# Kernel optimization log

Measured on AMD Instinct MI355X. Metric: run time of the kernel, lower is better.

Reference implementation:

```python
import jax, jax.numpy as jnp
import numpy as np

EMB = 1024
SHARED_MLP = 2048
MOE_MLP = 1024
N_EXPERTS = 8
TOP_K = 2
EPS = 1e-6


def rms_norm(x, scale=None, eps=EPS):
    # MaxText RMSNorm: x * rsqrt(mean(x^2)+eps) [* scale]
    y = x * jax.lax.rsqrt(jnp.mean(jnp.square(x), axis=-1, keepdims=True) + eps)
    return y if scale is None else y * scale


def setup_inputs() -> dict:
    key = jax.random.key(0)
    ks = jax.random.split(key, 12)
    B, S, D, F, M, E = 2, 2048, EMB, SHARED_MLP, MOE_MLP, N_EXPERTS
    sd = D ** -0.5
    sm = M ** -0.5
    sf = F ** -0.5
    return {
        "inputs": jax.random.normal(ks[0], (B, S, D), jnp.float32),
        "original_inputs": jax.random.normal(ks[1], (B, S, D), jnp.float32),
        # norm scales (init ~ ones with small perturbation for non-trivial math)
        "pre_forward_scale": 1.0 + 0.02 * jax.random.normal(ks[2], (D,), jnp.float32),
        "pre_ff_ln2_scale": 1.0 + 0.02 * jax.random.normal(ks[3], (D,), jnp.float32),
        "post_ff_ln1_scale": 1.0 + 0.02 * jax.random.normal(ks[4], (D,), jnp.float32),
        "post_ff_ln2_scale": 1.0 + 0.02 * jax.random.normal(ks[5], (D,), jnp.float32),
        # router and routed expert weights
        "router_w": jax.random.normal(ks[6], (D, E), jnp.float32) * sd,
        "e_wi0": jax.random.normal(ks[7], (E, D, M), jnp.float32) * sd,
        "e_wi1": jax.random.normal(ks[8], (E, D, M), jnp.float32) * sd,
        "e_wo": jax.random.normal(ks[9], (E, M, D), jnp.float32) * sm,
        # shared expert (gated MLP)
        "s_wi0": jax.random.normal(ks[10], (D, F), jnp.float32) * sd,
        "s_wi1": jax.random.normal(ks[11], (D, F), jnp.float32) * sd,
        "s_wo": jax.random.normal(jax.random.fold_in(key, 99), (F, D), jnp.float32) * sf,
    }


def _forward(inputs, original_inputs, pre_forward_scale, pre_ff_ln2_scale,
             post_ff_ln1_scale, post_ff_ln2_scale, router_w,
             e_wi0, e_wi1, e_wo, s_wi0, s_wi1, s_wo):
    B, S, D = inputs.shape
    E, K = N_EXPERTS, TOP_K
    # ---- shared experts: gated GeLU MLP on `inputs` ----
    h_sh = jax.nn.gelu(jnp.einsum('bsd,df->bsf', inputs, s_wi0)) * \
           jnp.einsum('bsd,df->bsf', inputs, s_wi1)
    shared = jnp.einsum('bsf,fd->bsd', h_sh, s_wo)
    shared = rms_norm(shared, post_ff_ln1_scale)
    # ---- gate-norm scaling (no-scale RMSNorm * emb^-0.5 * learned scale) ----
    routed_in = rms_norm(original_inputs, pre_ff_ln2_scale)
    gate_in = rms_norm(original_inputs) * (D ** -0.5) * pre_forward_scale  # f32 gate
    # ---- routing: softmax logits, top-k, renormalized combine weights ----
    logits = jnp.einsum('bsd,de->bse', gate_in.astype(jnp.float32), router_w)
    probs = jax.nn.softmax(logits, axis=-1)                       # [B,S,E]
    top_w, top_i = jax.lax.top_k(probs, K)                        # [B,S,K]
    top_w = top_w / jnp.sum(top_w, axis=-1, keepdims=True)
    onehot = jax.nn.one_hot(top_i, E, dtype=probs.dtype)          # [B,S,K,E]
    combine = jnp.einsum('bske,bsk->bse', onehot, top_w)          # [B,S,E]
    # ---- dropless routed experts: dense per-expert gated FFN + weighted combine ----
    x = routed_in.reshape(B * S, D)                               # [T,D]
    cw = combine.reshape(B * S, E)                                # [T,E]
    h = jax.nn.gelu(jnp.einsum('td,edm->etm', x, e_wi0)) * \
        jnp.einsum('td,edm->etm', x, e_wi1)                       # [E,T,M]
    routed = jnp.einsum('etm,emd,te->td', h, e_wo, cw)            # [T,D]
    routed = rms_norm(routed.reshape(B, S, D), post_ff_ln2_scale)
    # ---- load-balance aux loss (switch-style) ----
    frac_tokens = jnp.mean(jnp.sum(onehot, axis=-2), axis=(0, 1)) / K  # [E]
    frac_probs = jnp.mean(probs, axis=(0, 1))                          # [E]
    lb_loss = E * jnp.sum(frac_tokens * frac_probs)
    return routed + shared, lb_loss


def reference(inputs, original_inputs, pre_forward_scale, pre_ff_ln2_scale,
              post_ff_ln1_scale, post_ff_ln2_scale, router_w,
              e_wi0, e_wi1, e_wo, s_wi0, s_wi1, s_wo):
    out, lb_loss = _forward(inputs, original_inputs, pre_forward_scale,
                            pre_ff_ln2_scale, post_ff_ln1_scale, post_ff_ln2_scale,
                            router_w, e_wi0, e_wi1, e_wo, s_wi0, s_wi1, s_wo)
    return out, lb_loss
```

## Files before the change

kernel.cpp:

```cpp
#include <hip/hip_runtime.h>
#include <stdint.h>


typedef unsigned short u16;
typedef u16 u16x4 __attribute__((ext_vector_type(4)));
typedef u16 u16x8 __attribute__((ext_vector_type(8)));
typedef _Float16 f16x8 __attribute__((ext_vector_type(8)));
typedef float f32x4 __attribute__((ext_vector_type(4)));
typedef __attribute__((address_space(1))) void* as1_vp;
typedef __attribute__((address_space(3))) void* as3_vp;

#define T_TOK 4096
#define DIM   1024
#define FDIM  2048
#define MDIM  1024
#define NEXP  8
#define MAXTILES 72
#define HROWS (MAXTILES * 128)

__device__ __forceinline__ u16 f2h(float f) {
  _Float16 h = (_Float16)f;
  return __builtin_bit_cast(u16, h);
}
__device__ __forceinline__ float h2f(u16 u) {
  return (float)__builtin_bit_cast(_Float16, u);
}
__device__ __forceinline__ float gelu_f(float x) {
  const float y2 = x * (1.5957691216f + 0.0713548163f * x * x);
  return x / (1.0f + __expf(-y2));
}
__device__ __forceinline__ void async_copy16(const void* g, void* l) {
  __builtin_amdgcn_global_load_lds((as1_vp)(uintptr_t)g,
                                   (as3_vp)(uint32_t)(uintptr_t)l, 16, 0, 0);
}
__device__ __forceinline__ f16x8 lds_frag(const u16* p) {
  return __builtin_bit_cast(f16x8, *(const u16x8*)p);
}

__global__ __launch_bounds__(256, 2) void gemm_in(
    const u16* __restrict__ xs, const u16* __restrict__ swi_t,
    const u16* __restrict__ routed, const u16* __restrict__ ewi_t,
    u16* __restrict__ Hs, u16* __restrict__ Hr,
    const int* __restrict__ ridx, const int2* __restrict__ tdesc,
    const int* __restrict__ n_tiles) {
  const int yb = (int)blockIdx.y;
  const u16 *A, *B0t, *B1t;
  u16* H;
  int N;
  long bm;
  bool gather;
  if (yb < 32) {
    bm = (long)yb * 128;
    A = xs;
    B0t = swi_t;
    B1t = swi_t + (size_t)FDIM * DIM;
    H = Hs;
    N = FDIM;
    gather = false;
  } else {
    const int ty = yb - 32;
    if (ty >= *n_tiles) return;
    if ((int)blockIdx.x >= MDIM / 128) return;
    const int2 td = tdesc[ty];
    bm = td.y;
    A = routed;
    B0t = ewi_t + (long)td.x * MDIM * DIM;
    B1t = ewi_t + (size_t)NEXP * MDIM * DIM + (long)td.x * MDIM * DIM;
    H = Hr;
    N = MDIM;
    gather = true;
  }
  __shared__ __align__(16) u16 As[128 * 64];
  __shared__ __align__(16) u16 Bs0[128 * 64];
  __shared__ __align__(16) u16 Bs1[128 * 64];
  const int tid = threadIdx.x;
  const int lane = tid & 63;
  const int wave = tid >> 6;
  const int wm = (wave >> 1) * 64;
  const int wn = (wave & 1) * 64;
  const long bn = (long)blockIdx.x * 128;

  f32x4 acc0[4][4] = {}, acc1[4][4] = {};

  const int r0 = tid >> 3;
  const int cc = ((tid & 7) ^ (r0 & 7)) * 8;
  const long rowstride = 32 * (long)DIM;
  const u16* Ag[4];
  if (gather) {
#pragma unroll
    for (int i = 0; i < 4; i++) Ag[i] = A + (long)ridx[bm + r0 + i * 32] * DIM + cc;
  } else {
#pragma unroll
    for (int i = 0; i < 4; i++) Ag[i] = A + (bm + r0 + i * 32) * (long)DIM + cc;
  }
  const u16* B0g = B0t + (bn + r0) * (long)DIM + cc;
  const u16* B1g = B1t + (bn + r0) * (long)DIM + cc;
  const int fr = lane & 15;
  const int fq = lane >> 4;

  for (int k0 = 0; k0 < DIM; k0 += 64) {
#pragma unroll
    for (int i = 0; i < 4; i++) {
      async_copy16(Ag[i] + k0, &As[tid * 8 + i * 2048]);
      async_copy16(B0g + i * rowstride + k0, &Bs0[tid * 8 + i * 2048]);
      async_copy16(B1g + i * rowstride + k0, &Bs1[tid * 8 + i * 2048]);
    }
    __syncthreads();
#pragma unroll
    for (int kc = 0; kc < 8; kc += 4) {
      f16x8 af[4], b0[4], b1[4];
      const int q = (fq + kc) ^ (fr & 7);
#pragma unroll
      for (int i = 0; i < 4; i++) {
        af[i] = lds_frag(&As[(wm + i * 16 + fr) * 64 + q * 8]);
        b0[i] = lds_frag(&Bs0[(wn + i * 16 + fr) * 64 + q * 8]);
        b1[i] = lds_frag(&Bs1[(wn + i * 16 + fr) * 64 + q * 8]);
      }
#pragma unroll
      for (int mi = 0; mi < 4; mi++)
#pragma unroll
        for (int ni = 0; ni < 4; ni++) {
          acc0[mi][ni] = __builtin_amdgcn_mfma_f32_16x16x32_f16(af[mi], b0[ni], acc0[mi][ni], 0, 0, 0);
          acc1[mi][ni] = __builtin_amdgcn_mfma_f32_16x16x32_f16(af[mi], b1[ni], acc1[mi][ni], 0, 0, 0);
        }
    }
    __syncthreads();
  }

  const int er = (lane >> 4) * 4;
  const int ec = lane & 15;
#pragma unroll
  for (int mi = 0; mi < 4; mi++)
#pragma unroll
    for (int r = 0; r < 4; r++) {
      const long row = bm + wm + mi * 16 + er + r;
#pragma unroll
      for (int ni = 0; ni < 4; ni++)
        H[row * N + bn + wn + ni * 16 + ec] =
            f2h(gelu_f(acc0[mi][ni][r]) * acc1[mi][ni][r]);
    }
}

__global__ __launch_bounds__(256) void gemm_out2(
    const u16* __restrict__ Hs, const u16* __restrict__ swo_t,
    float* __restrict__ racc, const u16* __restrict__ Hr,
    const u16* __restrict__ ewo_t, float* __restrict__ Hout,
    const int2* __restrict__ tdesc, const int* __restrict__ n_tiles) {
  const int yb = (int)blockIdx.y;
  const u16 *A, *Bt;
  float* C;
  long bm;
  int K;
  if (yb < 32) {
    bm = (long)yb * 128;
    A = Hs;
    Bt = swo_t;
    K = FDIM;
    C = racc;
  } else {
    const int ty = yb - 32;
    if (ty >= *n_tiles) return;
    const int2 td = tdesc[ty];
    bm = td.y;
    A = Hr;
    Bt = ewo_t + (long)td.x * DIM * MDIM;
    K = MDIM;
    C = Hout;
  }
  __shared__ __align__(16) u16 As[128 * 64];
  __shared__ __align__(16) u16 Bs[128 * 64];
  const int tid = threadIdx.x;
  const int lane = tid & 63;
  const int wave = tid >> 6;
  const int wm = (wave >> 1) * 64;
  const int wn = (wave & 1) * 64;
  const long bn = (long)blockIdx.x * 128;

  f32x4 acc[4][4] = {};
  const int r0 = tid >> 3;
  const int cc = ((tid & 7) ^ (r0 & 7)) * 8;
  const long rowstride = 32 * (long)K;
  const u16* Ag[4];
#pragma unroll
  for (int i = 0; i < 4; i++) Ag[i] = A + (bm + r0 + i * 32) * (long)K + cc;
  const u16* Bg = Bt + (bn + r0) * (long)K + cc;
  const int fr = lane & 15;
  const int fq = lane >> 4;

  for (int k0 = 0; k0 < K; k0 += 64) {
#pragma unroll
    for (int i = 0; i < 4; i++) {
      async_copy16(Ag[i] + k0, &As[tid * 8 + i * 2048]);
      async_copy16(Bg + i * rowstride + k0, &Bs[tid * 8 + i * 2048]);
    }
    __syncthreads();
#pragma unroll
    for (int kc = 0; kc < 8; kc += 4) {
      f16x8 af[4], bq[4];
      const int q = (fq + kc) ^ (fr & 7);
#pragma unroll
      for (int i = 0; i < 4; i++) {
        af[i] = lds_frag(&As[(wm + i * 16 + fr) * 64 + q * 8]);
        bq[i] = lds_frag(&Bs[(wn + i * 16 + fr) * 64 + q * 8]);
      }
#pragma unroll
      for (int mi = 0; mi < 4; mi++)
#pragma unroll
        for (int ni = 0; ni < 4; ni++)
          acc[mi][ni] = __builtin_amdgcn_mfma_f32_16x16x32_f16(af[mi], bq[ni], acc[mi][ni], 0, 0, 0);
    }
    __syncthreads();
  }

  const int er = (lane >> 4) * 4;
  const int ec = lane & 15;
#pragma unroll
  for (int mi = 0; mi < 4; mi++)
#pragma unroll
    for (int r = 0; r < 4; r++) {
      const long row = bm + wm + mi * 16 + er + r;
#pragma unroll
      for (int ni = 0; ni < 4; ni++)
        C[row * DIM + bn + wn + ni * 16 + ec] = acc[mi][ni][r];
    }
}

__global__ __launch_bounds__(256) void transpose_cvt2(
    const float* __restrict__ s0, const float* __restrict__ s1,
    u16* __restrict__ dst, int R, int C, int zsplit) {
  __shared__ float tile[64][65];
  const int z = blockIdx.z;
  const float* src = (z < zsplit) ? s0 + (size_t)z * R * C
                                  : s1 + (size_t)(z - zsplit) * R * C;
  u16* d = dst + (size_t)z * R * C;
  const int c0 = blockIdx.x * 64, r0 = blockIdx.y * 64;
  const int tx = (threadIdx.x & 15) * 4;
  const int ty = threadIdx.x >> 4;
#pragma unroll
  for (int p = 0; p < 4; p++) {
    const float4 v =
        *(const float4*)(src + (size_t)(r0 + ty + p * 16) * C + c0 + tx);
    tile[ty + p * 16][tx + 0] = v.x;
    tile[ty + p * 16][tx + 1] = v.y;
    tile[ty + p * 16][tx + 2] = v.z;
    tile[ty + p * 16][tx + 3] = v.w;
  }
  __syncthreads();
  const int or8 = (threadIdx.x & 7) * 8;
  const int oc = threadIdx.x >> 3;
#pragma unroll
  for (int p = 0; p < 2; p++) {
    const int c = oc + p * 32;
    u16x8 o;
#pragma unroll
    for (int j = 0; j < 8; j++) o[j] = f2h(tile[or8 + j][c]);
    *(u16x8*)(d + (size_t)(c0 + c) * R + r0 + or8) = o;
  }
}

__global__ __launch_bounds__(256) void router_kernel(
    const float* __restrict__ orig, const float* __restrict__ inputs,
    const float* __restrict__ pfs, const float* __restrict__ ln2s,
    const float* __restrict__ rw, u16* __restrict__ routed_in,
    u16* __restrict__ x_sh, int* __restrict__ eidx, float* __restrict__ ewt,
    float* __restrict__ probs_out) {
  const int t = blockIdx.x;
  const int tid = threadIdx.x;
  const int d = tid * 4;
  {
    const float4 xi = *(const float4*)(inputs + (long)t * DIM + d);
    u16x4 xo = {f2h(xi.x), f2h(xi.y), f2h(xi.z), f2h(xi.w)};
    *(u16x4*)(x_sh + (long)t * DIM + d) = xo;
  }
  const float4 v = *(const float4*)(orig + (long)t * DIM + d);
  float ss = v.x * v.x + v.y * v.y + v.z * v.z + v.w * v.w;
#pragma unroll
  for (int off = 32; off > 0; off >>= 1) ss += __shfl_down(ss, off);
  __shared__ float red[4];
  __shared__ float lred[4][8];
  if ((tid & 63) == 0) red[tid >> 6] = ss;
  __syncthreads();
  const float rs = rsqrtf((red[0] + red[1] + red[2] + red[3]) * (1.0f / DIM) + 1e-6f);

  const float4 l2 = *(const float4*)(ln2s + d);
  u16x4 ro = {f2h(v.x * rs * l2.x), f2h(v.y * rs * l2.y), f2h(v.z * rs * l2.z),
              f2h(v.w * rs * l2.w)};
  *(u16x4*)(routed_in + (long)t * DIM + d) = ro;

  const float4 pf = *(const float4*)(pfs + d);
  const float c = rs * 0.03125f;
  const float g0 = v.x * c * pf.x, g1 = v.y * c * pf.y;
  const float g2 = v.z * c * pf.z, g3 = v.w * c * pf.w;
  float lg[8];
#pragma unroll
  for (int e = 0; e < 8; e++)
    lg[e] = g0 * rw[(d + 0) * 8 + e] + g1 * rw[(d + 1) * 8 + e] +
            g2 * rw[(d + 2) * 8 + e] + g3 * rw[(d + 3) * 8 + e];
#pragma unroll
  for (int e = 0; e < 8; e++)
#pragma unroll
    for (int off = 32; off > 0; off >>= 1) lg[e] += __shfl_down(lg[e], off);
  if ((tid & 63) == 0)
#pragma unroll
    for (int e = 0; e < 8; e++) lred[tid >> 6][e] = lg[e];
  __syncthreads();
  if (tid == 0) {
    float lz[8], p[8];
    float mx = -1e30f;
#pragma unroll
    for (int e = 0; e < 8; e++) {
      lz[e] = lred[0][e] + lred[1][e] + lred[2][e] + lred[3][e];
      mx = fmaxf(mx, lz[e]);
    }
    float s = 0.0f;
#pragma unroll
    for (int e = 0; e < 8; e++) {
      p[e] = expf(lz[e] - mx);
      s += p[e];
    }
    const float invs = 1.0f / s;
#pragma unroll
    for (int e = 0; e < 8; e++) p[e] *= invs;
    int i1 = 0;
    for (int e = 1; e < 8; e++)
      if (p[e] > p[i1]) i1 = e;
    int i2 = (i1 == 0) ? 1 : 0;
    for (int e = 0; e < 8; e++)
      if (e != i1 && p[e] > p[i2]) i2 = e;
    const float wsum = p[i1] + p[i2];
    eidx[2 * t] = i1;
    eidx[2 * t + 1] = i2;
    ewt[2 * t] = p[i1] / wsum;
    ewt[2 * t + 1] = p[i2] / wsum;
    float* prow = probs_out + (long)t * 8;
    for (int e = 0; e < 8; e++) prow[e] = p[e];
  }
}

__global__ __launch_bounds__(256) void bucket_count(const int* __restrict__ eidx,
                                                    int* __restrict__ counts) {
  __shared__ int lcnt[8];
  const int tid = threadIdx.x;
  if (tid < 8) lcnt[tid] = 0;
  __syncthreads();
  const int t = blockIdx.x * 256 + tid;
  atomicAdd(&lcnt[eidx[2 * t]], 1);
  atomicAdd(&lcnt[eidx[2 * t + 1]], 1);
  __syncthreads();
  if (tid < 8) atomicAdd(&counts[tid], lcnt[tid]);
}

__global__ void setup_tiles(const int* __restrict__ counts, int* __restrict__ poffset,
                            int2* __restrict__ tdesc, int* __restrict__ n_tiles) {
  if (threadIdx.x == 0 && blockIdx.x == 0) {
    int cur = 0, nt = 0;
    for (int e = 0; e < NEXP; e++) {
      poffset[e] = cur;
      const int ntile = (counts[e] + 127) >> 7;
      for (int i = 0; i < ntile; i++) {
        int2 d;
        d.x = e;
        d.y = cur + i * 128;
        tdesc[nt++] = d;
      }
      cur += ntile * 128;
    }
    n_tiles[0] = nt;
  }
}

__global__ __launch_bounds__(256) void bucket_scatter(
    const int* __restrict__ eidx, const int* __restrict__ poffset,
    int* __restrict__ cursors, int* __restrict__ ridx, int* __restrict__ pos) {
  __shared__ int lcnt[8], base[8];
  const int tid = threadIdx.x;
  if (tid < 8) lcnt[tid] = 0;
  __syncthreads();
  const int t = blockIdx.x * 256 + tid;
  const int e0 = eidx[2 * t], e1 = eidx[2 * t + 1];
  const int r0 = atomicAdd(&lcnt[e0], 1);
  const int r1 = atomicAdd(&lcnt[e1], 1);
  __syncthreads();
  if (tid < 8) base[tid] = atomicAdd(&cursors[tid], lcnt[tid]);
  __syncthreads();
  const int p0 = poffset[e0] + base[e0] + r0;
  const int p1 = poffset[e1] + base[e1] + r1;
  ridx[p0] = t;
  ridx[p1] = t;
  pos[2 * t] = p0;
  pos[2 * t + 1] = p1;
}

__global__ __launch_bounds__(256) void lb_reduce(const float* __restrict__ probs,
                                                 const int* __restrict__ counts,
                                                 float* __restrict__ out) {
  const int tid = threadIdx.x;
  float psum[8] = {};
  for (int tt = 0; tt < 16; tt++) {
    const long t = (long)tid * 16 + tt;
    const float4* pp = (const float4*)(probs + t * 8);
    const float4 p0 = pp[0], p1 = pp[1];
    psum[0] += p0.x; psum[1] += p0.y; psum[2] += p0.z; psum[3] += p0.w;
    psum[4] += p1.x; psum[5] += p1.y; psum[6] += p1.z; psum[7] += p1.w;
  }
#pragma unroll
  for (int e = 0; e < 8; e++)
#pragma unroll
    for (int off = 32; off > 0; off >>= 1) psum[e] += __shfl_down(psum[e], off);
  __shared__ float sp[4][8];
  if ((tid & 63) == 0)
#pragma unroll
    for (int e = 0; e < 8; e++) sp[tid >> 6][e] = psum[e];
  __syncthreads();
  if (tid == 0) {
    float loss = 0.0f;
#pragma unroll
    for (int e = 0; e < 8; e++) {
      const float fp = (sp[0][e] + sp[1][e] + sp[2][e] + sp[3][e]) / 4096.0f;
      const float ft = (float)counts[e] / (4096.0f * 2.0f);
      loss += ft * fp;
    }
    out[0] = 8.0f * loss;
  }
}

__global__ __launch_bounds__(256) void final_norm(
    const float* __restrict__ racc, const float* __restrict__ Hout,
    const int* __restrict__ pos, const float* __restrict__ ewt,
    const float* __restrict__ post1, const float* __restrict__ post2,
    float* __restrict__ out) {
  const int t = blockIdx.x;
  const int tid = threadIdx.x;
  const int d = tid * 4;
  const long base = (long)t * DIM + d;
  const float4 vs = *(const float4*)(racc + base);
  const float w0 = ewt[2 * t], w1 = ewt[2 * t + 1];
  const long p0 = pos[2 * t], p1 = pos[2 * t + 1];
  const float4 a0 = *(const float4*)(Hout + p0 * DIM + d);
  const float4 b0 = *(const float4*)(Hout + p1 * DIM + d);
  float4 vr;
  vr.x = w0 * a0.x + w1 * b0.x;
  vr.y = w0 * a0.y + w1 * b0.y;
  vr.z = w0 * a0.z + w1 * b0.z;
  vr.w = w0 * a0.w + w1 * b0.w;
  float ss = vs.x * vs.x + vs.y * vs.y + vs.z * vs.z + vs.w * vs.w;
  float sr = vr.x * vr.x + vr.y * vr.y + vr.z * vr.z + vr.w * vr.w;
#pragma unroll
  for (int off = 32; off > 0; off >>= 1) {
    ss += __shfl_down(ss, off);
    sr += __shfl_down(sr, off);
  }
  __shared__ float reds[4], redr[4];
  if ((tid & 63) == 0) {
    reds[tid >> 6] = ss;
    redr[tid >> 6] = sr;
  }
  __syncthreads();
  const float rss = rsqrtf((reds[0] + reds[1] + reds[2] + reds[3]) * (1.0f / DIM) + 1e-6f);
  const float rsr = rsqrtf((redr[0] + redr[1] + redr[2] + redr[3]) * (1.0f / DIM) + 1e-6f);
  const float4 s1 = *(const float4*)(post1 + d);
  const float4 s2 = *(const float4*)(post2 + d);
  float4 o;
  o.x = vs.x * rss * s1.x + vr.x * rsr * s2.x;
  o.y = vs.y * rss * s1.y + vr.y * rsr * s2.y;
  o.z = vs.z * rss * s1.z + vr.z * rsr * s2.z;
  o.w = vs.w * rss * s1.w + vr.w * rsr * s2.w;
  *(float4*)(out + base) = o;
}

extern "C" void kernel_launch(void* const* d_in, const int* in_sizes, int n_in,
                              void* d_out, int out_size, void* d_ws, size_t ws_size,
                              hipStream_t stream) {
  (void)in_sizes; (void)n_in; (void)out_size; (void)ws_size;
  const float* inputs   = (const float*)d_in[0];
  const float* orig     = (const float*)d_in[1];
  const float* pfs      = (const float*)d_in[2];
  const float* ln2s     = (const float*)d_in[3];
  const float* post1    = (const float*)d_in[4];
  const float* post2    = (const float*)d_in[5];
  const float* router_w = (const float*)d_in[6];
  const float* e_wi0    = (const float*)d_in[7];
  const float* e_wi1    = (const float*)d_in[8];
  const float* e_wo     = (const float*)d_in[9];
  const float* s_wi0    = (const float*)d_in[10];
  const float* s_wi1    = (const float*)d_in[11];
  const float* s_wo     = (const float*)d_in[12];

  char* ws = (char*)d_ws;
  size_t o = 0;
  auto alloc = [&](size_t bytes) -> void* {
    void* p = ws + o;
    o += (bytes + 255) & ~(size_t)255;
    return p;
  };
  u16* s_wi_t  = (u16*)alloc((size_t)2 * FDIM * DIM * 2);
  u16* s_wo_t  = (u16*)alloc((size_t)DIM * FDIM * 2);
  u16* e_wi_t  = (u16*)alloc((size_t)2 * NEXP * MDIM * DIM * 2);
  u16* e_wo_t  = (u16*)alloc((size_t)NEXP * DIM * MDIM * 2);
  u16* x_sh    = (u16*)alloc((size_t)T_TOK * DIM * 2);
  u16* routed  = (u16*)alloc((size_t)T_TOK * DIM * 2);
  float* probs = (float*)alloc((size_t)T_TOK * 8 * 4);
  int* eidx    = (int*)alloc((size_t)T_TOK * 2 * 4);
  float* ewt   = (float*)alloc((size_t)T_TOK * 2 * 4);
  int* pos     = (int*)alloc((size_t)T_TOK * 2 * 4);
  int* imeta   = (int*)alloc(256);
  int* poffset = (int*)alloc(64);
  int* n_tiles = (int*)alloc(64);
  int2* tdesc  = (int2*)alloc(MAXTILES * 8);
  int* ridx    = (int*)alloc((size_t)HROWS * 4);
  float* racc  = (float*)alloc((size_t)T_TOK * DIM * 4);
  u16* Hs      = (u16*)alloc((size_t)T_TOK * FDIM * 2);
  u16* H       = (u16*)alloc((size_t)HROWS * MDIM * 2);
  float* Hout  = (float*)alloc((size_t)HROWS * DIM * 4);

  int* counts = imeta;
  int* cursors = imeta + 8;

  hipMemsetAsync(imeta, 0, 64, stream);
  hipMemsetAsync(ridx, 0, (size_t)HROWS * 4, stream);

  transpose_cvt2<<<dim3(FDIM / 64, DIM / 64, 2), 256, 0, stream>>>(
      s_wi0, s_wi1, s_wi_t, DIM, FDIM, 1);
  transpose_cvt2<<<dim3(DIM / 64, FDIM / 64, 1), 256, 0, stream>>>(
      s_wo, s_wo, s_wo_t, FDIM, DIM, 1);
  transpose_cvt2<<<dim3(MDIM / 64, DIM / 64, 16), 256, 0, stream>>>(
      e_wi0, e_wi1, e_wi_t, DIM, MDIM, 8);
  transpose_cvt2<<<dim3(DIM / 64, MDIM / 64, 8), 256, 0, stream>>>(
      e_wo, e_wo, e_wo_t, MDIM, DIM, 8);

  router_kernel<<<T_TOK, 256, 0, stream>>>(orig, inputs, pfs, ln2s, router_w,
                                           routed, x_sh, eidx, ewt, probs);

  bucket_count<<<16, 256, 0, stream>>>(eidx, counts);
  setup_tiles<<<1, 64, 0, stream>>>(counts, poffset, tdesc, n_tiles);
  bucket_scatter<<<16, 256, 0, stream>>>(eidx, poffset, cursors, ridx, pos);

  gemm_in<<<dim3(FDIM / 128, 32 + MAXTILES, 1), 256, 0, stream>>>(
      x_sh, s_wi_t, routed, e_wi_t, Hs, H, ridx, tdesc, n_tiles);

  gemm_out2<<<dim3(DIM / 128, 32 + MAXTILES, 1), 256, 0, stream>>>(
      Hs, s_wo_t, racc, H, e_wo_t, Hout, tdesc, n_tiles);

  final_norm<<<T_TOK, 256, 0, stream>>>(racc, Hout, pos, ewt, post1, post2,
                                        (float*)d_out);

  lb_reduce<<<1, 256, 0, stream>>>(probs, counts, (float*)d_out + (size_t)T_TOK * DIM);
}
```

Before: 423.5 us.

## Merge launches: single transpose, one-wave-per-token router, fused bucketing, lb into final_norm

Combines the four weight transpose launches into one flat-grid kernel and merges bucket_count, setup_tiles and bucket_scatter into a single 512-thread block. The block also zero-fills the padding rows of ridx, which replaces both memsets. The router now handles one token per wavefront with 16 elements per lane, so it needs no LDS reductions or block barriers. The load-balance reduction moves into an extra block of final_norm. Together these cut the launch count and sync overhead, at the cost of serializing the bucketing onto one block.

```diff
diff --git a/kernel.cpp b/kernel.cpp
--- a/kernel.cpp
+++ b/kernel.cpp
@@ -22,9 +22,6 @@
   _Float16 h = (_Float16)f;
   return __builtin_bit_cast(u16, h);
 }
-__device__ __forceinline__ float h2f(u16 u) {
-  return (float)__builtin_bit_cast(_Float16, u);
-}
 __device__ __forceinline__ float gelu_f(float x) {
   const float y2 = x * (1.5957691216f + 0.0713548163f * x * x);
   return x / (1.0f + __expf(-y2));
@@ -35,6 +32,12 @@
 }
 __device__ __forceinline__ f16x8 lds_frag(const u16* p) {
   return __builtin_bit_cast(f16x8, *(const u16x8*)p);
+}
+__device__ __forceinline__ u16x8 pack8(float4 a, float4 b) {
+  u16x8 o;
+  o[0] = f2h(a.x); o[1] = f2h(a.y); o[2] = f2h(a.z); o[3] = f2h(a.w);
+  o[4] = f2h(b.x); o[5] = f2h(b.y); o[6] = f2h(b.z); o[7] = f2h(b.w);
+  return o;
 }
 
 __global__ __launch_bounds__(256, 2) void gemm_in(
@@ -225,25 +228,55 @@
     }
 }
 
-__global__ __launch_bounds__(256) void transpose_cvt2(
-    const float* __restrict__ s0, const float* __restrict__ s1,
-    u16* __restrict__ dst, int R, int C, int zsplit) {
-  __shared__ float tile[64][65];
-  const int z = blockIdx.z;
-  const float* src = (z < zsplit) ? s0 + (size_t)z * R * C
-                                  : s1 + (size_t)(z - zsplit) * R * C;
-  u16* d = dst + (size_t)z * R * C;
-  const int c0 = blockIdx.x * 64, r0 = blockIdx.y * 64;
+__global__ __launch_bounds__(256) void transpose_all(
+    const float* __restrict__ s_wi0, const float* __restrict__ s_wi1,
+    const float* __restrict__ s_wo, const float* __restrict__ e_wi0,
+    const float* __restrict__ e_wi1, const float* __restrict__ e_wo,
+    u16* __restrict__ s_wi_t, u16* __restrict__ s_wo_t,
+    u16* __restrict__ e_wi_t, u16* __restrict__ e_wo_t) {
+  const int b = (int)blockIdx.x;
+  const float* src;
+  u16* dst;
+  int R, C, tile;
+  if (b < 1024) {
+    const int z = b >> 9;
+    tile = b & 511;
+    src = z ? s_wi1 : s_wi0;
+    dst = s_wi_t + (size_t)z * FDIM * DIM;
+    R = DIM; C = FDIM;
+  } else if (b < 1536) {
+    tile = b - 1024;
+    src = s_wo;
+    dst = s_wo_t;
+    R = FDIM; C = DIM;
+  } else if (b < 5632) {
+    const int z = (b - 1536) >> 8;
+    tile = b & 255;
+    src = (z < 8) ? e_wi0 + (size_t)z * DIM * MDIM
+                  : e_wi1 + (size_t)(z - 8) * DIM * MDIM;
+    dst = e_wi_t + (size_t)z * MDIM * DIM;
+    R = DIM; C = MDIM;
+  } else {
+    const int z = (b - 5632) >> 8;
+    tile = b & 255;
+    src = e_wo + (size_t)z * MDIM * DIM;
+    dst = e_wo_t + (size_t)z * DIM * MDIM;
+    R = MDIM; C = DIM;
+  }
+  const int ctiles = C >> 6;
+  const int c0 = (tile % ctiles) * 64, r0 = (tile / ctiles) * 64;
+
+  __shared__ float tl[64][65];
   const int tx = (threadIdx.x & 15) * 4;
   const int ty = threadIdx.x >> 4;
 #pragma unroll
   for (int p = 0; p < 4; p++) {
     const float4 v =
         *(const float4*)(src + (size_t)(r0 + ty + p * 16) * C + c0 + tx);
-    tile[ty + p * 16][tx + 0] = v.x;
-    tile[ty + p * 16][tx + 1] = v.y;
-    tile[ty + p * 16][tx + 2] = v.z;
-    tile[ty + p * 16][tx + 3] = v.w;
+    tl[ty + p * 16][tx + 0] = v.x;
+    tl[ty + p * 16][tx + 1] = v.y;
+    tl[ty + p * 16][tx + 2] = v.z;
+    tl[ty + p * 16][tx + 3] = v.w;
   }
   __syncthreads();
   const int or8 = (threadIdx.x & 7) * 8;
@@ -253,8 +286,8 @@
     const int c = oc + p * 32;
     u16x8 o;
 #pragma unroll
-    for (int j = 0; j < 8; j++) o[j] = f2h(tile[or8 + j][c]);
-    *(u16x8*)(d + (size_t)(c0 + c) * R + r0 + or8) = o;
+    for (int j = 0; j < 8; j++) o[j] = f2h(tl[or8 + j][c]);
+    *(u16x8*)(dst + (size_t)(c0 + c) * R + r0 + or8) = o;
   }
 }
 
@@ -264,58 +297,84 @@
     const float* __restrict__ rw, u16* __restrict__ routed_in,
     u16* __restrict__ x_sh, int* __restrict__ eidx, float* __restrict__ ewt,
     float* __restrict__ probs_out) {
-  const int t = blockIdx.x;
-  const int tid = threadIdx.x;
-  const int d = tid * 4;
+  const int wv = threadIdx.x >> 6;
+  const int lane = threadIdx.x & 63;
+  const int t = blockIdx.x * 4 + wv;
+  const int d0 = lane * 16;
+  const size_t base = (size_t)t * DIM + d0;
+
+  const float4 v0 = *(const float4*)(orig + base);
+  const float4 v1 = *(const float4*)(orig + base + 4);
+  const float4 v2 = *(const float4*)(orig + base + 8);
+  const float4 v3 = *(const float4*)(orig + base + 12);
   {
-    const float4 xi = *(const float4*)(inputs + (long)t * DIM + d);
-    u16x4 xo = {f2h(xi.x), f2h(xi.y), f2h(xi.z), f2h(xi.w)};
-    *(u16x4*)(x_sh + (long)t * DIM + d) = xo;
-  }
-  const float4 v = *(const float4*)(orig + (long)t * DIM + d);
-  float ss = v.x * v.x + v.y * v.y + v.z * v.z + v.w * v.w;
+    const float4 x0 = *(const float4*)(inputs + base);
+    const float4 x1 = *(const float4*)(inputs + base + 4);
+    const float4 x2 = *(const float4*)(inputs + base + 8);
+    const float4 x3 = *(const float4*)(inputs + base + 12);
+    *(u16x8*)(x_sh + base) = pack8(x0, x1);
+    *(u16x8*)(x_sh + base + 8) = pack8(x2, x3);
+  }
+  float ss = v0.x * v0.x + v0.y * v0.y + v0.z * v0.z + v0.w * v0.w +
+             v1.x * v1.x + v1.y * v1.y + v1.z * v1.z + v1.w * v1.w +
+             v2.x * v2.x + v2.y * v2.y + v2.z * v2.z + v2.w * v2.w +
+             v3.x * v3.x + v3.y * v3.y + v3.z * v3.z + v3.w * v3.w;
 #pragma unroll
   for (int off = 32; off > 0; off >>= 1) ss += __shfl_down(ss, off);
-  __shared__ float red[4];
-  __shared__ float lred[4][8];
-  if ((tid & 63) == 0) red[tid >> 6] = ss;
-  __syncthreads();
-  const float rs = rsqrtf((red[0] + red[1] + red[2] + red[3]) * (1.0f / DIM) + 1e-6f);
-
-  const float4 l2 = *(const float4*)(ln2s + d);
-  u16x4 ro = {f2h(v.x * rs * l2.x), f2h(v.y * rs * l2.y), f2h(v.z * rs * l2.z),
-              f2h(v.w * rs * l2.w)};
-  *(u16x4*)(routed_in + (long)t * DIM + d) = ro;
-
-  const float4 pf = *(const float4*)(pfs + d);
+  ss = __shfl(ss, 0);
+  const float rs = rsqrtf(ss * (1.0f / DIM) + 1e-6f);
+
+  {
+    const float4 l0 = *(const float4*)(ln2s + d0);
+    const float4 l1 = *(const float4*)(ln2s + d0 + 4);
+    const float4 l2 = *(const float4*)(ln2s + d0 + 8);
+    const float4 l3 = *(const float4*)(ln2s + d0 + 12);
+    float4 r0c, r1c, r2c, r3c;
+    r0c.x = v0.x * rs * l0.x; r0c.y = v0.y * rs * l0.y;
+    r0c.z = v0.z * rs * l0.z; r0c.w = v0.w * rs * l0.w;
+    r1c.x = v1.x * rs * l1.x; r1c.y = v1.y * rs * l1.y;
+    r1c.z = v1.z * rs * l1.z; r1c.w = v1.w * rs * l1.w;
+    r2c.x = v2.x * rs * l2.x; r2c.y = v2.y * rs * l2.y;
+    r2c.z = v2.z * rs * l2.z; r2c.w = v2.w * rs * l2.w;
+    r3c.x = v3.x * rs * l3.x; r3c.y = v3.y * rs * l3.y;
+    r3c.z = v3.z * rs * l3.z; r3c.w = v3.w * rs * l3.w;
+    *(u16x8*)(routed_in + base) = pack8(r0c, r1c);
+    *(u16x8*)(routed_in + base + 8) = pack8(r2c, r3c);
+  }
+
+  const float4 p0 = *(const float4*)(pfs + d0);
+  const float4 p1 = *(const float4*)(pfs + d0 + 4);
+  const float4 p2 = *(const float4*)(pfs + d0 + 8);
+  const float4 p3 = *(const float4*)(pfs + d0 + 12);
   const float c = rs * 0.03125f;
-  const float g0 = v.x * c * pf.x, g1 = v.y * c * pf.y;
-  const float g2 = v.z * c * pf.z, g3 = v.w * c * pf.w;
-  float lg[8];
+  const float g[16] = {v0.x * c * p0.x, v0.y * c * p0.y, v0.z * c * p0.z, v0.w * c * p0.w,
+                       v1.x * c * p1.x, v1.y * c * p1.y, v1.z * c * p1.z, v1.w * c * p1.w,
+                       v2.x * c * p2.x, v2.y * c * p2.y, v2.z * c * p2.z, v2.w * c * p2.w,
+                       v3.x * c * p3.x, v3.y * c * p3.y, v3.z * c * p3.z, v3.w * c * p3.w};
+  float lg[8] = {};
+#pragma unroll
+  for (int j = 0; j < 16; j++) {
+    const float4 ra = *(const float4*)(rw + (size_t)(d0 + j) * 8);
+    const float4 rb = *(const float4*)(rw + (size_t)(d0 + j) * 8 + 4);
+    lg[0] += g[j] * ra.x; lg[1] += g[j] * ra.y;
+    lg[2] += g[j] * ra.z; lg[3] += g[j] * ra.w;
+    lg[4] += g[j] * rb.x; lg[5] += g[j] * rb.y;
+    lg[6] += g[j] * rb.z; lg[7] += g[j] * rb.w;
+  }
 #pragma unroll
   for (int e = 0; e < 8; e++)
-    lg[e] = g0 * rw[(d + 0) * 8 + e] + g1 * rw[(d + 1) * 8 + e] +
-            g2 * rw[(d + 2) * 8 + e] + g3 * rw[(d + 3) * 8 + e];
-#pragma unroll
-  for (int e = 0; e < 8; e++)
 #pragma unroll
     for (int off = 32; off > 0; off >>= 1) lg[e] += __shfl_down(lg[e], off);
-  if ((tid & 63) == 0)
-#pragma unroll
-    for (int e = 0; e < 8; e++) lred[tid >> 6][e] = lg[e];
-  __syncthreads();
-  if (tid == 0) {
-    float lz[8], p[8];
+
+  if (lane == 0) {
+    float p[8];
     float mx = -1e30f;
 #pragma unroll
+    for (int e = 0; e < 8; e++) mx = fmaxf(mx, lg[e]);
+    float s = 0.0f;
+#pragma unroll
     for (int e = 0; e < 8; e++) {
-      lz[e] = lred[0][e] + lred[1][e] + lred[2][e] + lred[3][e];
-      mx = fmaxf(mx, lz[e]);
-    }
-    float s = 0.0f;
-#pragma unroll
-    for (int e = 0; e < 8; e++) {
-      p[e] = expf(lz[e] - mx);
+      p[e] = expf(lg[e] - mx);
       s += p[e];
     }
     const float invs = 1.0f / s;
@@ -332,31 +391,30 @@
     eidx[2 * t + 1] = i2;
     ewt[2 * t] = p[i1] / wsum;
     ewt[2 * t + 1] = p[i2] / wsum;
-    float* prow = probs_out + (long)t * 8;
+    float* prow = probs_out + (size_t)t * 8;
     for (int e = 0; e < 8; e++) prow[e] = p[e];
   }
 }
 
-__global__ __launch_bounds__(256) void bucket_count(const int* __restrict__ eidx,
-                                                    int* __restrict__ counts) {
-  __shared__ int lcnt[8];
+__global__ __launch_bounds__(512) void bucket_all(
+    const int* __restrict__ eidx, int* __restrict__ counts_g,
+    int2* __restrict__ tdesc, int* __restrict__ n_tiles,
+    int* __restrict__ ridx, int* __restrict__ pos) {
+  __shared__ int cnt[8], off[8], cursor[8];
   const int tid = threadIdx.x;
-  if (tid < 8) lcnt[tid] = 0;
+  if (tid < 8) {
+    cnt[tid] = 0;
+    cursor[tid] = 0;
+  }
   __syncthreads();
-  const int t = blockIdx.x * 256 + tid;
-  atomicAdd(&lcnt[eidx[2 * t]], 1);
-  atomicAdd(&lcnt[eidx[2 * t + 1]], 1);
+  for (int i = tid; i < 2 * T_TOK; i += 512) atomicAdd(&cnt[eidx[i]], 1);
   __syncthreads();
-  if (tid < 8) atomicAdd(&counts[tid], lcnt[tid]);
-}
-
-__global__ void setup_tiles(const int* __restrict__ counts, int* __restrict__ poffset,
-                            int2* __restrict__ tdesc, int* __restrict__ n_tiles) {
-  if (threadIdx.x == 0 && blockIdx.x == 0) {
+  if (tid == 0) {
     int cur = 0, nt = 0;
     for (int e = 0; e < NEXP; e++) {
-      poffset[e] = cur;
-      const int ntile = (counts[e] + 127) >> 7;
+      off[e] = cur;
+      counts_g[e] = cnt[e];
+      const int ntile = (cnt[e] + 127) >> 7;
       for (int i = 0; i < ntile; i++) {
         int2 d;
         d.x = e;
@@ -367,60 +425,20 @@
     }
     n_tiles[0] = nt;
   }
-}
-
-__global__ __launch_bounds__(256) void bucket_scatter(
-    const int* __restrict__ eidx, const int* __restrict__ poffset,
-    int* __restrict__ cursors, int* __restrict__ ridx, int* __restrict__ pos) {
-  __shared__ int lcnt[8], base[8];
-  const int tid = threadIdx.x;
-  if (tid < 8) lcnt[tid] = 0;
   __syncthreads();
-  const int t = blockIdx.x * 256 + tid;
-  const int e0 = eidx[2 * t], e1 = eidx[2 * t + 1];
-  const int r0 = atomicAdd(&lcnt[e0], 1);
-  const int r1 = atomicAdd(&lcnt[e1], 1);
+  for (int i = tid; i < 2 * T_TOK; i += 512) {
+    const int e = eidx[i];
+    const int r = atomicAdd(&cursor[e], 1);
+    const int p = off[e] + r;
+    ridx[p] = i >> 1;
+    pos[i] = p;
+  }
   __syncthreads();
-  if (tid < 8) base[tid] = atomicAdd(&cursors[tid], lcnt[tid]);
-  __syncthreads();
-  const int p0 = poffset[e0] + base[e0] + r0;
-  const int p1 = poffset[e1] + base[e1] + r1;
-  ridx[p0] = t;
-  ridx[p1] = t;
-  pos[2 * t] = p0;
-  pos[2 * t + 1] = p1;
-}
-
-__global__ __launch_bounds__(256) void lb_reduce(const float* __restrict__ probs,
-                                                 const int* __restrict__ counts,
-                                                 float* __restrict__ out) {
-  const int tid = threadIdx.x;
-  float psum[8] = {};
-  for (int tt = 0; tt < 16; tt++) {
-    const long t = (long)tid * 16 + tt;
-    const float4* pp = (const float4*)(probs + t * 8);
-    const float4 p0 = pp[0], p1 = pp[1];
-    psum[0] += p0.x; psum[1] += p0.y; psum[2] += p0.z; psum[3] += p0.w;
-    psum[4] += p1.x; psum[5] += p1.y; psum[6] += p1.z; psum[7] += p1.w;
-  }
-#pragma unroll
-  for (int e = 0; e < 8; e++)
-#pragma unroll
-    for (int off = 32; off > 0; off >>= 1) psum[e] += __shfl_down(psum[e], off);
-  __shared__ float sp[4][8];
-  if ((tid & 63) == 0)
-#pragma unroll
-    for (int e = 0; e < 8; e++) sp[tid >> 6][e] = psum[e];
-  __syncthreads();
-  if (tid == 0) {
-    float loss = 0.0f;
-#pragma unroll
-    for (int e = 0; e < 8; e++) {
-      const float fp = (sp[0][e] + sp[1][e] + sp[2][e] + sp[3][e]) / 4096.0f;
-      const float ft = (float)counts[e] / (4096.0f * 2.0f);
-      loss += ft * fp;
-    }
-    out[0] = 8.0f * loss;
+#pragma unroll
+  for (int e = 0; e < NEXP; e++) {
+    const int s = off[e] + cnt[e];
+    const int en = off[e] + (((cnt[e] + 127) >> 7) << 7);
+    for (int i = s + tid; i < en; i += 512) ridx[i] = 0;
   }
 }
 
@@ -428,9 +446,40 @@
     const float* __restrict__ racc, const float* __restrict__ Hout,
     const int* __restrict__ pos, const float* __restrict__ ewt,
     const float* __restrict__ post1, const float* __restrict__ post2,
-    float* __restrict__ out) {
+    float* __restrict__ out, const float* __restrict__ probs,
+    const int* __restrict__ counts) {
+  const int tid = threadIdx.x;
+  if (blockIdx.x == T_TOK) {
+    float psum[8] = {};
+    for (int tt = 0; tt < 16; tt++) {
+      const long t = (long)tid * 16 + tt;
+      const float4* pp = (const float4*)(probs + t * 8);
+      const float4 p0 = pp[0], p1 = pp[1];
+      psum[0] += p0.x; psum[1] += p0.y; psum[2] += p0.z; psum[3] += p0.w;
+      psum[4] += p1.x; psum[5] += p1.y; psum[6] += p1.z; psum[7] += p1.w;
+    }
+#pragma unroll
+    for (int e = 0; e < 8; e++)
+#pragma unroll
+      for (int off = 32; off > 0; off >>= 1) psum[e] += __shfl_down(psum[e], off);
+    __shared__ float sp[4][8];
+    if ((tid & 63) == 0)
+#pragma unroll
+      for (int e = 0; e < 8; e++) sp[tid >> 6][e] = psum[e];
+    __syncthreads();
+    if (tid == 0) {
+      float loss = 0.0f;
+#pragma unroll
+      for (int e = 0; e < 8; e++) {
+        const float fp = (sp[0][e] + sp[1][e] + sp[2][e] + sp[3][e]) / 4096.0f;
+        const float ft = (float)counts[e] / (4096.0f * 2.0f);
+        loss += ft * fp;
+      }
+      out[(size_t)T_TOK * DIM] = 8.0f * loss;
+    }
+    return;
+  }
   const int t = blockIdx.x;
-  const int tid = threadIdx.x;
   const int d = tid * 4;
   const long base = (long)t * DIM + d;
   const float4 vs = *(const float4*)(racc + base);
@@ -504,7 +553,6 @@
   float* ewt   = (float*)alloc((size_t)T_TOK * 2 * 4);
   int* pos     = (int*)alloc((size_t)T_TOK * 2 * 4);
   int* imeta   = (int*)alloc(256);
-  int* poffset = (int*)alloc(64);
   int* n_tiles = (int*)alloc(64);
   int2* tdesc  = (int2*)alloc(MAXTILES * 8);
   int* ridx    = (int*)alloc((size_t)HROWS * 4);
@@ -514,26 +562,15 @@
   float* Hout  = (float*)alloc((size_t)HROWS * DIM * 4);
 
   int* counts = imeta;
-  int* cursors = imeta + 8;
-
-  hipMemsetAsync(imeta, 0, 64, stream);
-  hipMemsetAsync(ridx, 0, (size_t)HROWS * 4, stream);
-
-  transpose_cvt2<<<dim3(FDIM / 64, DIM / 64, 2), 256, 0, stream>>>(
-      s_wi0, s_wi1, s_wi_t, DIM, FDIM, 1);
-  transpose_cvt2<<<dim3(DIM / 64, FDIM / 64, 1), 256, 0, stream>>>(
-      s_wo, s_wo, s_wo_t, FDIM, DIM, 1);
-  transpose_cvt2<<<dim3(MDIM / 64, DIM / 64, 16), 256, 0, stream>>>(
-      e_wi0, e_wi1, e_wi_t, DIM, MDIM, 8);
-  transpose_cvt2<<<dim3(DIM / 64, MDIM / 64, 8), 256, 0, stream>>>(
-      e_wo, e_wo, e_wo_t, MDIM, DIM, 8);
-
-  router_kernel<<<T_TOK, 256, 0, stream>>>(orig, inputs, pfs, ln2s, router_w,
-                                           routed, x_sh, eidx, ewt, probs);
-
-  bucket_count<<<16, 256, 0, stream>>>(eidx, counts);
-  setup_tiles<<<1, 64, 0, stream>>>(counts, poffset, tdesc, n_tiles);
-  bucket_scatter<<<16, 256, 0, stream>>>(eidx, poffset, cursors, ridx, pos);
+
+  transpose_all<<<7680, 256, 0, stream>>>(s_wi0, s_wi1, s_wo, e_wi0, e_wi1,
+                                          e_wo, s_wi_t, s_wo_t, e_wi_t, e_wo_t);
+
+  router_kernel<<<T_TOK / 4, 256, 0, stream>>>(orig, inputs, pfs, ln2s,
+                                               router_w, routed, x_sh, eidx,
+                                               ewt, probs);
+
+  bucket_all<<<1, 512, 0, stream>>>(eidx, counts, tdesc, n_tiles, ridx, pos);
 
   gemm_in<<<dim3(FDIM / 128, 32 + MAXTILES, 1), 256, 0, stream>>>(
       x_sh, s_wi_t, routed, e_wi_t, Hs, H, ridx, tdesc, n_tiles);
@@ -541,8 +578,6 @@
   gemm_out2<<<dim3(DIM / 128, 32 + MAXTILES, 1), 256, 0, stream>>>(
       Hs, s_wo_t, racc, H, e_wo_t, Hout, tdesc, n_tiles);
 
-  final_norm<<<T_TOK, 256, 0, stream>>>(racc, Hout, pos, ewt, post1, post2,
-                                        (float*)d_out);
-
-  lb_reduce<<<1, 256, 0, stream>>>(probs, counts, (float*)d_out + (size_t)T_TOK * DIM);
-}
+  final_norm<<<T_TOK + 1, 256, 0, stream>>>(racc, Hout, pos, ewt, post1, post2,
+                                            (float*)d_out, probs, counts);
+}
```

New measurement: 418.5 us. No clear change (-1.2%).
